# Optimization experiments

Measured on AMD Instinct MI355X. Metric: run time of the kernel, lower is better.

## Reference

```python
import jax, jax.numpy as jnp
import numpy as np

B, T, D = 2048, 200, 64
H1, H2 = 80, 40
CONST_MIN = -4294967295.0


def setup_inputs() -> dict:
    key = jax.random.key(0)
    ks = jax.random.split(key, 10)
    q = jax.random.normal(ks[0], (B, D), dtype=jnp.float32)
    k = jax.random.normal(ks[1], (B, T, D), dtype=jnp.float32)
    v = jax.random.normal(ks[2], (B, T, D), dtype=jnp.float32)
    mask = jax.random.randint(ks[3], (B, T), 0, 2, dtype=jnp.int32)
    # MLP params: Dense(80, sigmoid) -> Dense(40, sigmoid) -> Dense(1)
    s1 = 1.0 / np.sqrt(4 * D)
    W1 = jax.random.normal(ks[4], (4 * D, H1), dtype=jnp.float32) * s1
    b1 = jnp.zeros((H1,), dtype=jnp.float32)
    W2 = jax.random.normal(ks[5], (H1, H2), dtype=jnp.float32) * (1.0 / np.sqrt(H1))
    b2 = jnp.zeros((H2,), dtype=jnp.float32)
    Wf = jax.random.normal(ks[6], (H2, 1), dtype=jnp.float32) * (1.0 / np.sqrt(H2))
    bf = jnp.zeros((1,), dtype=jnp.float32)
    return {"q": q, "k": k, "v": v, "mask": mask,
            "W1": W1, "b1": b1, "W2": W2, "b2": b2, "Wf": Wf, "bf": bf}


def reference(q, k, v, mask, W1, b1, W2, b2, Wf, bf):
    # q: [B,D] tiled over T -> [B,T,D]
    qt = jnp.broadcast_to(q[:, None, :], k.shape)
    # per-pair features [B,T,4D]
    info = jnp.concatenate([qt, k, qt - k, qt * k], axis=-1)
    h = jax.nn.sigmoid(jnp.einsum('btf,fh->bth', info, W1) + b1)
    h = jax.nn.sigmoid(jnp.einsum('bth,hg->btg', h, W2) + b2)
    logits = (jnp.einsum('btg,go->bto', h, Wf) + bf)[..., 0]  # [B,T]
    logits = jnp.where(mask == 0, jnp.float32(CONST_MIN), logits)
    w = jax.nn.softmax(logits, axis=-1)  # [B,T]
    out = jnp.einsum('bt,btd->bd', w, v)  # weighted sum of v
    return out
```

## Files before the change

### kernel.cpp

```cpp
#include <hip/hip_runtime.h>
#include <math.h>

#define T_LEN 200

typedef short bf8 __attribute__((ext_vector_type(8)));
typedef float f32x4 __attribute__((ext_vector_type(4)));

__device__ __forceinline__ float sigmoidf_(float x){ return 1.0f/(1.0f+__expf(-x)); }
__device__ __forceinline__ unsigned int pk_bf16(float lo, float hi){
  unsigned int r; asm("v_cvt_pk_bf16_f32 %0, %1, %2":"=v"(r):"v"(lo),"v"(hi)); return r;
}
union U4B8 { uint4 u; bf8 b; };
__device__ __forceinline__ bf8 pack8(float4 x, float4 y){
  U4B8 r;
  r.u.x = pk_bf16(x.x,x.y); r.u.y = pk_bf16(x.z,x.w);
  r.u.z = pk_bf16(y.x,y.y); r.u.w = pk_bf16(y.z,y.w);
  return r.b;
}
__device__ __forceinline__ bf8 pack8m(float4 x, float4 qx, float4 y, float4 qy){
  U4B8 r;
  r.u.x = pk_bf16(x.x*qx.x, x.y*qx.y); r.u.y = pk_bf16(x.z*qx.z, x.w*qx.w);
  r.u.z = pk_bf16(y.x*qy.x, y.y*qy.y); r.u.w = pk_bf16(y.z*qy.z, y.w*qy.w);
  return r.b;
}

__global__ void prep_kernel(const float* __restrict__ W1, const float* __restrict__ W2,
                            const float* __restrict__ b2, const float* __restrict__ Wf,
                            float* __restrict__ wsf){
  unsigned short* fb = (unsigned short*)wsf;
  int i = blockIdx.x*256 + threadIdx.x;
  if (i < 15360){
    int fi = i >> 9;
    int lane = (i>>3)&63, e = i&7;
    int ht = fi/6, ks = fi%6;
    int h = ht*16 + (lane&15);
    int f = ks*32 + ((lane>>4)<<3) + e;
    float val;
    if (f < 64)        val = W1[(64+f)*80+h] - W1[(128+f)*80+h];
    else if (f < 128)  val = W1[(128+f)*80+h];
    else               val = W1[(f-128)*80+h] + W1[f*80+h];
    fb[i] = (unsigned short)(pk_bf16(val,val) & 0xffffu);
  }
  if (i < 4608){
    int fi = i >> 9;
    int lane = (i>>3)&63, e = i&7;
    int gt = fi/3, ks = fi%3;
    int g = gt*16 + (lane&15);
    int h = ks*32 + ((lane>>4)<<3) + e;
    float val = (g<40 && h<80) ? W2[h*40+g] : 0.f;
    fb[15360+i] = (unsigned short)(pk_bf16(val,val) & 0xffffu);
  }
  if (i < 48){
    wsf[9984  + i] = (i<40) ? b2[i] : 0.f;
    wsf[10032 + i] = (i<40) ? Wf[i] : 0.f;
  }
}

__global__ __launch_bounds__(64, 1) void fused_kernel(
    const float* __restrict__ q, const float* __restrict__ k, const float* __restrict__ v,
    const int* __restrict__ mask, const float* __restrict__ b1,
    const float* __restrict__ bf, const float* __restrict__ wsf,
    float* __restrict__ out)
{
  __shared__ unsigned short tl[224];
  __shared__ __align__(16) unsigned int Hw[2][16*52];

  const int lane = threadIdx.x;
  const int lg = lane>>4, lc = lane&15;
  const long b = blockIdx.x;

  const float* kb = k + b*(T_LEN*64);
  const float* vb = v + b*(T_LEN*64);
  const int*   mb = mask + b*T_LEN;
  const float* qb = q + b*64;
  const unsigned short* fbg = (const unsigned short*)wsf;
  const bf8* A1f = (const bf8*)fbg;
  const bf8* A2f = (const bf8*)(fbg + 15360);
  const float* b2p = wsf + 9984;
  const float* wfp = wsf + 10032;

  { uint4 z = {0,0,0,0}; *(uint4*)(&Hw[lane>>5][((lane&31)>>1)*52 + 40 + (lane&1)*4]) = z; }

  bf8 wk[20];
  #pragma unroll
  for (int ht=0; ht<5; ++ht)
    #pragma unroll
    for (int j=0; j<4; ++j) wk[ht*4+j] = A1f[(ht*6+j)*64+lane];
  bf8 w2[9];
  #pragma unroll
  for (int i=0; i<9; ++i) w2[i] = A2f[i*64+lane];
  float b2v[12], wfv[12];
  #pragma unroll
  for (int gt=0; gt<3; ++gt){
    float4 bv = *(const float4*)(b2p + gt*16 + lg*4);
    float4 wv = *(const float4*)(wfp + gt*16 + lg*4);
    b2v[gt*4+0]=bv.x; b2v[gt*4+1]=bv.y; b2v[gt*4+2]=bv.z; b2v[gt*4+3]=bv.w;
    wfv[gt*4+0]=wv.x; wfv[gt*4+1]=wv.y; wfv[gt*4+2]=wv.z; wfv[gt*4+3]=wv.w;
  }

  f32x4 qacc[5];
  float4 qA0 = *(const float4*)(qb + lg*8);
  float4 qA1 = *(const float4*)(qb + lg*8 + 4);
  float4 qB0 = *(const float4*)(qb + 32 + lg*8);
  float4 qB1 = *(const float4*)(qb + 32 + lg*8 + 4);
  {
    bf8 fq0 = pack8(qA0,qA1);
    bf8 fq1 = pack8(qB0,qB1);
    #pragma unroll
    for (int ht=0; ht<5; ++ht){
      float4 bv = *(const float4*)(b1 + ht*16 + lg*4);
      qacc[ht][0]=bv.x; qacc[ht][1]=bv.y; qacc[ht][2]=bv.z; qacc[ht][3]=bv.w;
      qacc[ht] = __builtin_amdgcn_mfma_f32_16x16x32_bf16(A1f[(ht*6+4)*64+lane], fq0, qacc[ht],0,0,0);
      qacc[ht] = __builtin_amdgcn_mfma_f32_16x16x32_bf16(A1f[(ht*6+5)*64+lane], fq1, qacc[ht],0,0,0);
    }
  }
  const float bf0 = bf[0];

  int tot = 0;
  unsigned long long ltm = (1ull<<lane) - 1ull;
  #pragma unroll
  for (int c=0;c<4;++c){
    int t = c*64 + lane;
    bool f = (t < T_LEN) && (mb[t] != 0);
    unsigned long long bal = __ballot(f);
    if (f) tl[tot + (int)__popcll(bal & ltm)] = (unsigned short)t;
    tot += (int)__popcll(bal);
  }
  asm volatile("s_waitcnt lgkmcnt(0)" ::: "memory");
  __builtin_amdgcn_sched_barrier(0);

  if (tot == 0){
    float accv = 0.f;
    for (int t=0; t<T_LEN; ++t) accv += vb[t*64 + lane];
    out[b*64 + lane] = accv * (1.0f/(float)T_LEN);
    return;
  }

  int tp = tl[min(lc, tot-1)];
  const float* kr = kb + tp*64 + lg*8;
  float4 na0 = *(const float4*)(kr);
  float4 na1 = *(const float4*)(kr+4);
  float4 nb0 = *(const float4*)(kr+32);
  float4 nb1 = *(const float4*)(kr+36);

  float acc_pv0 = 0.f, acc_pv1 = 0.f;
  float se0 = 0.f, se1 = 0.f;
  int buf = 0;
  for (int base = 0; base < tot; base += 16, buf ^= 1){
    bf8 f0 = pack8(na0,na1);
    bf8 f1 = pack8(nb0,nb1);
    bf8 f2 = pack8m(na0,qA0,na1,qA1);
    bf8 f3 = pack8m(nb0,qB0,nb1,qB1);
    if (base + 16 < tot){
      int tn = tl[min(base+16+lc, tot-1)];
      const float* krn = kb + tn*64 + lg*8;
      na0 = *(const float4*)(krn);
      na1 = *(const float4*)(krn+4);
      nb0 = *(const float4*)(krn+32);
      nb1 = *(const float4*)(krn+36);
    }
    float vval[16];
    #pragma unroll
    for (int i=0;i<16;++i){
      int ti = tl[min(base+i, tot-1)];
      vval[i] = vb[ti*64 + lane];
    }

    f32x4 acc[5];
    #pragma unroll
    for (int ht=0; ht<5; ++ht) acc[ht] = qacc[ht];
    #pragma unroll
    for (int ht=0; ht<5; ++ht){
      acc[ht] = __builtin_amdgcn_mfma_f32_16x16x32_bf16(wk[ht*4+0], f0, acc[ht],0,0,0);
      acc[ht] = __builtin_amdgcn_mfma_f32_16x16x32_bf16(wk[ht*4+1], f1, acc[ht],0,0,0);
      acc[ht] = __builtin_amdgcn_mfma_f32_16x16x32_bf16(wk[ht*4+2], f2, acc[ht],0,0,0);
      acc[ht] = __builtin_amdgcn_mfma_f32_16x16x32_bf16(wk[ht*4+3], f3, acc[ht],0,0,0);
    }

    unsigned int* Hb = &Hw[buf][0];
    #pragma unroll
    for (int ht=0; ht<5; ++ht){
      #pragma unroll
      for (int rp=0; rp<2; ++rp)
        Hb[lc*52 + ht*8+lg*2+rp] = pk_bf16(sigmoidf_(acc[ht][2*rp]), sigmoidf_(acc[ht][2*rp+1]));
    }
    asm volatile("s_waitcnt lgkmcnt(0)" ::: "memory");
    __builtin_amdgcn_sched_barrier(0);

    bf8 c0[3];
    #pragma unroll
    for (int ks=0; ks<3; ++ks) c0[ks] = *(const bf8*)(Hb + lc*52 + 16*ks + 4*lg);
    f32x4 g0[3];
    #pragma unroll
    for (int gt=0; gt<3; ++gt){
      g0[gt][0]=b2v[gt*4+0]; g0[gt][1]=b2v[gt*4+1]; g0[gt][2]=b2v[gt*4+2]; g0[gt][3]=b2v[gt*4+3];
    }
    #pragma unroll
    for (int gt=0; gt<3; ++gt){
      #pragma unroll
      for (int ks=0; ks<3; ++ks)
        g0[gt] = __builtin_amdgcn_mfma_f32_16x16x32_bf16(w2[gt*3+ks], c0[ks], g0[gt],0,0,0);
    }
    float p0=0.f;
    #pragma unroll
    for (int gt=0; gt<3; ++gt){
      #pragma unroll
      for (int r=0;r<4;++r) p0 = fmaf(wfv[gt*4+r], sigmoidf_(g0[gt][r]), p0);
    }
    p0 += __shfl_xor(p0,16); p0 += __shfl_xor(p0,32);
    float e_own = (base+lc < tot) ? __expf(p0 + bf0) : 0.f;

    #pragma unroll
    for (int i=0;i<16;i+=2){
      float ei0 = __shfl(e_own, i);
      float ei1 = __shfl(e_own, i+1);
      se0 += ei0; se1 += ei1;
      acc_pv0 = fmaf(ei0, vval[i],   acc_pv0);
      acc_pv1 = fmaf(ei1, vval[i+1], acc_pv1);
    }
  }

  out[b*64 + lane] = (acc_pv0 + acc_pv1) / (se0 + se1);
}

extern "C" void kernel_launch(void* const* d_in, const int* in_sizes, int n_in,
                              void* d_out, int out_size, void* d_ws, size_t ws_size,
                              hipStream_t stream) {
  const float* q    = (const float*)d_in[0];
  const float* k    = (const float*)d_in[1];
  const float* v    = (const float*)d_in[2];
  const int*   mask = (const int*)d_in[3];
  const float* W1   = (const float*)d_in[4];
  const float* b1   = (const float*)d_in[5];
  const float* W2   = (const float*)d_in[6];
  const float* b2   = (const float*)d_in[7];
  const float* Wf   = (const float*)d_in[8];
  const float* bf   = (const float*)d_in[9];
  float* out = (float*)d_out;
  float* wsf = (float*)d_ws;

  hipLaunchKernelGGL(prep_kernel, dim3(60), dim3(256), 0, stream, W1, W2, b2, Wf, wsf);
  hipLaunchKernelGGL(fused_kernel, dim3(2048), dim3(64), 0, stream,
                     q, k, v, mask, b1, bf, wsf, out);
}
```

Measured before the change: 46.51 us.

## Prefetch next V rows, stage W2 fragments in LDS, broadcast exps via LDS

Moves the V-row gathers one iteration ahead so their latency overlaps the current chunk's MFMA work, using a double-buffered register array. Moves the W2 MFMA fragments from registers into shared memory to free VGPRs, at the cost of an extra LDS read per MFMA. Replaces the cross-lane shuffles that broadcast the softmax exponents with an LDS write followed by broadcast reads. Together these raise register pressure from the prefetch buffer while cutting it elsewhere, and add LDS traffic in the inner loop.

```diff
diff --git a/kernel.cpp b/kernel.cpp
--- a/kernel.cpp
+++ b/kernel.cpp
@@ -64,6 +64,8 @@
 {
   __shared__ unsigned short tl[224];
   __shared__ __align__(16) unsigned int Hw[2][16*52];
+  __shared__ float e_lds[16];
+  __shared__ __align__(16) unsigned int w2s[9*64*4];
 
   const int lane = threadIdx.x;
   const int lg = lane>>4, lc = lane&15;
@@ -75,20 +77,20 @@
   const float* qb = q + b*64;
   const unsigned short* fbg = (const unsigned short*)wsf;
   const bf8* A1f = (const bf8*)fbg;
-  const bf8* A2f = (const bf8*)(fbg + 15360);
+  const uint4* A2u = (const uint4*)(fbg + 15360);
   const float* b2p = wsf + 9984;
   const float* wfp = wsf + 10032;
 
   { uint4 z = {0,0,0,0}; *(uint4*)(&Hw[lane>>5][((lane&31)>>1)*52 + 40 + (lane&1)*4]) = z; }
 
+  #pragma unroll
+  for (int i=0;i<9;++i) ((uint4*)w2s)[i*64+lane] = A2u[i*64+lane];
+
   bf8 wk[20];
   #pragma unroll
   for (int ht=0; ht<5; ++ht)
     #pragma unroll
     for (int j=0; j<4; ++j) wk[ht*4+j] = A1f[(ht*6+j)*64+lane];
-  bf8 w2[9];
-  #pragma unroll
-  for (int i=0; i<9; ++i) w2[i] = A2f[i*64+lane];
   float b2v[12], wfv[12];
   #pragma unroll
   for (int gt=0; gt<3; ++gt){
@@ -142,28 +144,35 @@
   float4 na1 = *(const float4*)(kr+4);
   float4 nb0 = *(const float4*)(kr+32);
   float4 nb1 = *(const float4*)(kr+36);
+  float vcur[16];
+  #pragma unroll
+  for (int i=0;i<16;++i){
+    int ti = tl[min(i, tot-1)];
+    vcur[i] = vb[ti*64 + lane];
+  }
 
   float acc_pv0 = 0.f, acc_pv1 = 0.f;
   float se0 = 0.f, se1 = 0.f;
   int buf = 0;
   for (int base = 0; base < tot; base += 16, buf ^= 1){
+    const bool have_next = (base + 16 < tot);
     bf8 f0 = pack8(na0,na1);
     bf8 f1 = pack8(nb0,nb1);
     bf8 f2 = pack8m(na0,qA0,na1,qA1);
     bf8 f3 = pack8m(nb0,qB0,nb1,qB1);
-    if (base + 16 < tot){
+    float vnxt[16];
+    if (have_next){
       int tn = tl[min(base+16+lc, tot-1)];
       const float* krn = kb + tn*64 + lg*8;
       na0 = *(const float4*)(krn);
       na1 = *(const float4*)(krn+4);
       nb0 = *(const float4*)(krn+32);
       nb1 = *(const float4*)(krn+36);
-    }
-    float vval[16];
-    #pragma unroll
-    for (int i=0;i<16;++i){
-      int ti = tl[min(base+i, tot-1)];
-      vval[i] = vb[ti*64 + lane];
+      #pragma unroll
+      for (int i=0;i<16;++i){
+        int ti = tl[min(base+16+i, tot-1)];
+        vnxt[i] = vb[ti*64 + lane];
+      }
     }
 
     f32x4 acc[5];
@@ -198,8 +207,10 @@
     #pragma unroll
     for (int gt=0; gt<3; ++gt){
       #pragma unroll
-      for (int ks=0; ks<3; ++ks)
-        g0[gt] = __builtin_amdgcn_mfma_f32_16x16x32_bf16(w2[gt*3+ks], c0[ks], g0[gt],0,0,0);
+      for (int ks=0; ks<3; ++ks){
+        bf8 wf2 = *(const bf8*)(w2s + ((gt*3+ks)*64+lane)*4);
+        g0[gt] = __builtin_amdgcn_mfma_f32_16x16x32_bf16(wf2, c0[ks], g0[gt],0,0,0);
+      }
     }
     float p0=0.f;
     #pragma unroll
@@ -208,15 +219,21 @@
       for (int r=0;r<4;++r) p0 = fmaf(wfv[gt*4+r], sigmoidf_(g0[gt][r]), p0);
     }
     p0 += __shfl_xor(p0,16); p0 += __shfl_xor(p0,32);
-    float e_own = (base+lc < tot) ? __expf(p0 + bf0) : 0.f;
+    if (lg == 0) e_lds[lc] = (base+lc < tot) ? __expf(p0 + bf0) : 0.f;
+    asm volatile("s_waitcnt lgkmcnt(0)" ::: "memory");
+    __builtin_amdgcn_sched_barrier(0);
 
     #pragma unroll
     for (int i=0;i<16;i+=2){
-      float ei0 = __shfl(e_own, i);
-      float ei1 = __shfl(e_own, i+1);
+      float ei0 = e_lds[i];
+      float ei1 = e_lds[i+1];
       se0 += ei0; se1 += ei1;
-      acc_pv0 = fmaf(ei0, vval[i],   acc_pv0);
-      acc_pv1 = fmaf(ei1, vval[i+1], acc_pv1);
+      acc_pv0 = fmaf(ei0, vcur[i],   acc_pv0);
+      acc_pv1 = fmaf(ei1, vcur[i+1], acc_pv1);
+    }
+    if (have_next){
+      #pragma unroll
+      for (int i=0;i<16;++i) vcur[i] = vnxt[i];
     }
   }
 
```

New measurement: 39.47 us. -15.1%, faster.
